# Kernel tuning notes

Measured on AMD Instinct MI355X. Metric: run time of the kernel, lower is better.

The kernel has to match this reference:

```python
import jax, jax.numpy as jnp
import numpy as np

B, C_IN, C_OUT, H, W, K, NK = 16, 256, 256, 64, 64, 3, 2
EPS = 1e-8


def setup_inputs() -> dict:
    key = jax.random.key(0)
    k1, k2, k3, k4 = jax.random.split(key, 4)
    x = jax.random.normal(k1, (B, C_IN, H, W), dtype=jnp.float32)
    mod = jax.random.normal(k2, (B, C_IN), dtype=jnp.float32)
    kernel_mod = jax.random.normal(k3, (B, NK), dtype=jnp.float32)
    # kernel bank: [num_conv_kernels, dim_out, dim_in, k, k] (kaiming-ish scale)
    weights = jax.random.normal(k4, (NK, C_OUT, C_IN, K, K), dtype=jnp.float32) / np.sqrt(C_IN * K * K)
    gamma = jnp.ones((C_OUT,), dtype=jnp.float32)
    return {"x": x, "mod": mod, "kernel_mod": kernel_mod, "weights": weights, "gamma": gamma}


def _block(x, mod, kernel_mod, weights, gamma):
    # adaptive kernel selection: softmax-mix the kernel bank per sample
    attn = jax.nn.softmax(kernel_mod, axis=-1)                       # [b, n]
    w = jnp.einsum('bn,noikl->boikl', attn, weights)                 # [b, o, i, k, k]
    # style modulation over input channels
    w = w * (mod[:, None, :, None, None] + 1.0)
    # demodulation
    denom = jnp.clip(jnp.sum(w * w, axis=(2, 3, 4), keepdims=True), EPS)
    w = w * jax.lax.rsqrt(denom)
    # per-sample conv (groups=b trick in torch) -> vmap over batch
    def conv_one(fmap, wb):
        return jax.lax.conv_general_dilated(
            fmap[None], wb, window_strides=(1, 1), padding='SAME',
            dimension_numbers=('NCHW', 'OIHW', 'NCHW'))[0]
    y = jax.vmap(conv_one)(x, w)                                     # [b, o, h, w]
    # RMSNorm over channel dim: F.normalize(x, dim=1) * gamma * sqrt(dim)
    norm = jnp.sqrt(jnp.sum(y * y, axis=1, keepdims=True))
    y = y / jnp.maximum(norm, 1e-12)
    y = y * gamma[None, :, None, None] * (gamma.shape[0] ** 0.5)
    # SiLU
    return y * jax.nn.sigmoid(y)


def reference(x, mod, kernel_mod, weights, gamma):
    return _block(x, mod, kernel_mod, weights, gamma)
```

## Files before the change

kernel.cpp:

```cpp
#include <hip/hip_runtime.h>
#include <math.h>


typedef __attribute__((ext_vector_type(8))) short short8;
typedef __attribute__((ext_vector_type(4))) float f32x4;

#define GLL16(src, dst)                                                       \
  __builtin_amdgcn_global_load_lds(                                           \
      (const __attribute__((address_space(1))) unsigned int*)(src),           \
      (__attribute__((address_space(3))) unsigned int*)(dst), 16, 0, 0)

static __device__ __forceinline__ unsigned short f2bf(float v) {
  union { float f; unsigned u; } u;
  u.f = v;
  unsigned r = u.u + 0x7FFF + ((u.u >> 16) & 1);
  return (unsigned short)(r >> 16);
}

__global__ __launch_bounds__(256) void scale_kernel(
    const float* __restrict__ mod, const float* __restrict__ kmod,
    const float* __restrict__ weights, float* __restrict__ scale) {
  int bo = blockIdx.x;
  int b = bo >> 8, o = bo & 255;

  float k0 = kmod[b * 2 + 0], k1 = kmod[b * 2 + 1];
  float mx = fmaxf(k0, k1);
  float e0 = expf(k0 - mx), e1 = expf(k1 - mx);
  float ai = 1.0f / (e0 + e1);
  float a0 = e0 * ai, a1 = e1 * ai;

  int t = threadIdx.x;
  const float* w0 = weights + (size_t)o * 2304;
  const float* w1 = w0 + 589824;

  float s = 0.0f;
#pragma unroll
  for (int r = 0; r < 9; r++) {
    int idx = t + r * 256;
    int i = idx / 9;
    float wv = a0 * w0[idx] + a1 * w1[idx];
    wv *= (mod[b * 256 + i] + 1.0f);
    s += wv * wv;
  }
#pragma unroll
  for (int off = 32; off > 0; off >>= 1) s += __shfl_down(s, off);

  __shared__ float red[4];
  if ((t & 63) == 0) red[t >> 6] = s;
  __syncthreads();
  if (t == 0) {
    float tot = red[0] + red[1] + red[2] + red[3];
    scale[bo] = rsqrtf(fmaxf(tot, 1e-8f));
  }
}

__global__ __launch_bounds__(256) void wprep(
    const float* __restrict__ mod, const float* __restrict__ kmod,
    const float* __restrict__ weights, const float* __restrict__ scale,
    unsigned short* __restrict__ wq) {
  __shared__ __align__(16) unsigned short buf[20480];
  int blk = blockIdx.x;
  int b = blk >> 5, ot = (blk >> 4) & 1, c = blk & 15;
  int t = threadIdx.x;

  float k0 = kmod[b * 2 + 0], k1 = kmod[b * 2 + 1];
  float mx = fmaxf(k0, k1);
  float e0 = expf(k0 - mx), e1 = expf(k1 - mx);
  float ai = 1.0f / (e0 + e1);
  float a0 = e0 * ai, a1 = e1 * ai;

#pragma unroll
  for (int k = 0; k < 8; ++k) {
    int e = t + k * 256;
    int half = e >> 10;
    buf[(half * 10 + 9) * 1024 + (e & 1023)] = 0;
  }

  int ol = t >> 1, eh = t & 1;
  int o = ot * 128 + ol;
  float sc = scale[b * 256 + o];
#pragma unroll
  for (int io = 0; io < 2; ++io) {
#pragma unroll
    for (int eo = 0; eo < 4; ++eo) {
      int e = eh * 4 + eo;
      int i = c * 16 + io * 8 + e;
      float f = (mod[b * 256 + i] + 1.0f) * sc;
      const float* w0 = &weights[((size_t)o * 256 + i) * 9];
      const float* w1 = w0 + 589824;
#pragma unroll
      for (int j = 0; j < 9; ++j) {
        float v = (a0 * w0[j] + a1 * w1[j]) * f;
        buf[(io * 10 + j) * 1024 + ol * 8 + e] = f2bf(v);
      }
    }
  }
  __syncthreads();
  size_t base = (size_t)blk * 20480;
#pragma unroll
  for (int k = 0; k < 10; ++k) {
    int idx = t + k * 256;
    *(short8*)(wq + base + (size_t)idx * 8) = *(const short8*)&buf[idx * 8];
  }
}

__global__ __launch_bounds__(256) void xprep(
    const float* __restrict__ x, unsigned short* __restrict__ xq) {
  int blk = blockIdx.x;
  int rowp = blk % 66;
  int bc = blk / 66;
  int b = bc >> 4, c = bc & 15;
  int t = threadIdx.x;
  size_t obase = (size_t)blk * 1056;

  if (rowp == 0 || rowp == 65) {
    for (int idx = t; idx < 1056; idx += 256) xq[obase + idx] = 0;
    return;
  }
  __shared__ __align__(16) unsigned short xs2[1056];
  int row = rowp - 1;
  for (int idx = t; idx < 1056; idx += 256) xs2[idx] = 0;
  __syncthreads();
#pragma unroll
  for (int k = 0; k < 4; ++k) {
    int idx = t + k * 256;
    int il = idx >> 6, col = idx & 63;
    float v = x[(((size_t)b * 256 + c * 16 + il) * 64 + row) * 64 + col];
    xs2[(col + 1) * 16 + il] = f2bf(v);
  }
  __syncthreads();
  if (t < 132) {
    int G = blk * 132 + t;
    int flip = ((G >> 3) & 1) ^ (bc & 1);
    *(short8*)(xq + obase + (size_t)(t ^ flip) * 8) = *(const short8*)&xs2[t * 8];
  }
}

__global__ __launch_bounds__(512, 2) void conv_mfma(
    const unsigned short* __restrict__ xq, const unsigned short* __restrict__ wq,
    float* __restrict__ out) {
  __shared__ __align__(16) unsigned short wsm[2][20480];
  __shared__ __align__(16) unsigned short xsm[2][10560];

  int bid = blockIdx.x;
  int xcd = bid & 7;
  int kk = bid >> 3;
  int b = xcd * 2 + (kk >> 4);
  int rem = kk & 15;
  int ot = rem >> 3;
  int rt = rem & 7;
  int r0 = rt * 8;

  int t = threadIdx.x;
  int w = t >> 6, lane = t & 63;
  int g = (t >> 4) & 3, lm = t & 15;

  int baddr_[5], aaddr_[5];
#pragma unroll
  for (int s = 0; s < 5; ++s) {
    int p = 4 * s + g;
    int io = (p >= 10) ? 1 : 0;
    int j = p - 10 * io;
    int jd3, jm3;
    if (j == 9) { jd3 = 0; jm3 = 0; }
    else { jd3 = (j >= 3) + (j >= 6); jm3 = j - 3 * jd3; }
    int ba = ((w + jd3) * 66 + lm + jm3) * 32 + io * 16;
    ba ^= ((ba >> 7) & 1) << 4;
    baddr_[s] = ba;
    aaddr_[s] = p * 2048 + lm * 16;
  }

  f32x4 acc[8][4];
#pragma unroll
  for (int mf = 0; mf < 8; ++mf)
#pragma unroll
    for (int nf = 0; nf < 4; ++nf) acc[mf][nf] = (f32x4){0.f, 0.f, 0.f, 0.f};

#define WGLL(cn, nb, r)                                                        \
  {                                                                            \
    const unsigned short* s_ = wq + ((size_t)(b * 32 + ot * 16 + (cn))) * 20480 \
                               + ((r) * 512 + w * 64 + lane) * 8;              \
    GLL16(s_, &wsm[nb][(r) * 4096 + w * 512]);                                 \
  }
#define XGLL(cn, nb, r)                                                        \
  {                                                                            \
    const unsigned short* s_ = xq + ((size_t)((b * 16 + (cn)) * 66 + r0)) * 1056 \
                               + ((r) * 512 + w * 64 + lane) * 8;              \
    GLL16(s_, &xsm[nb][(r) * 4096 + w * 512]);                                 \
  }

  WGLL(0, 0, 0); WGLL(0, 0, 1); WGLL(0, 0, 2); WGLL(0, 0, 3); WGLL(0, 0, 4);
  XGLL(0, 0, 0); XGLL(0, 0, 1);
  if (t < 296) XGLL(0, 0, 2);
  asm volatile("s_waitcnt vmcnt(0)" ::: "memory");
  __builtin_amdgcn_s_barrier();
  __builtin_amdgcn_sched_barrier(0);

  for (int c = 0; c < 16; ++c) {
    int cur = c & 1;
    const char* wsb = (const char*)wsm[cur];
    const char* xsb = (const char*)xsm[cur];
#pragma unroll
    for (int s = 0; s < 5; ++s) {
      if (c < 15) {
        int nb = cur ^ 1;
        if (s == 0) { WGLL(c + 1, nb, 0); WGLL(c + 1, nb, 1); XGLL(c + 1, nb, 0); }
        if (s == 1) { WGLL(c + 1, nb, 2); WGLL(c + 1, nb, 3); XGLL(c + 1, nb, 1); }
        if (s == 2) { WGLL(c + 1, nb, 4); if (t < 296) XGLL(c + 1, nb, 2); }
      }
      short8 A[8];
#pragma unroll
      for (int mf = 0; mf < 8; ++mf)
        A[mf] = *(const short8*)(wsb + aaddr_[s] + mf * 256);
      __builtin_amdgcn_s_setprio(1);
#pragma unroll
      for (int nf = 0; nf < 4; ++nf) {
        short8 Bf = *(const short8*)(xsb + baddr_[s] + nf * 512);
#pragma unroll
        for (int mf = 0; mf < 8; ++mf)
          acc[mf][nf] =
              __builtin_amdgcn_mfma_f32_16x16x32_bf16(A[mf], Bf, acc[mf][nf], 0, 0, 0);
      }
      __builtin_amdgcn_s_setprio(0);
    }
    asm volatile("s_waitcnt vmcnt(0)" ::: "memory");
    __builtin_amdgcn_s_barrier();
    __builtin_amdgcn_sched_barrier(0);
  }

  int row = r0 + w;
#pragma unroll
  for (int mf = 0; mf < 8; ++mf)
#pragma unroll
    for (int nf = 0; nf < 4; ++nf)
#pragma unroll
      for (int q = 0; q < 4; ++q) {
        int o = ot * 128 + mf * 16 + g * 4 + q;
        int col = nf * 16 + lm;
        out[(((size_t)b * 256 + o) * 64 + row) * 64 + col] = acc[mf][nf][q];
      }
#undef WGLL
#undef XGLL
}

__global__ __launch_bounds__(256) void norm_kernel(
    float* __restrict__ y, const float* __restrict__ gamma) {
  int blk = blockIdx.x;
  int b = blk >> 6, h = blk & 63;
  int t = threadIdx.x;
  int p = t & 63, og = t >> 6;

  size_t base = (((size_t)b * 256) * 64 + h) * 64 + p;
  float yv[64];
  float s = 0.0f;
#pragma unroll
  for (int k = 0; k < 64; k++) {
    yv[k] = y[base + (size_t)(og * 64 + k) * 4096];
    s = fmaf(yv[k], yv[k], s);
  }

  __shared__ float red[4][64];
  __shared__ float invs[64];
  red[og][p] = s;
  __syncthreads();
  if (og == 0) {
    float tot = red[0][p] + red[1][p] + red[2][p] + red[3][p];
    float nrm = sqrtf(tot);
    invs[p] = 16.0f / fmaxf(nrm, 1e-12f);
  }
  __syncthreads();
  float iv = invs[p];
#pragma unroll
  for (int k = 0; k < 64; k++) {
    int o = og * 64 + k;
    float v = yv[k] * iv * gamma[o];
    float sg = 1.0f / (1.0f + expf(-v));
    y[base + (size_t)o * 4096] = v * sg;
  }
}

extern "C" void kernel_launch(void* const* d_in, const int* in_sizes, int n_in,
                              void* d_out, int out_size, void* d_ws, size_t ws_size,
                              hipStream_t stream) {
  const float* x = (const float*)d_in[0];
  const float* mod = (const float*)d_in[1];
  const float* kmod = (const float*)d_in[2];
  const float* weights = (const float*)d_in[3];
  const float* gamma = (const float*)d_in[4];
  float* out = (float*)d_out;

  unsigned short* wq = (unsigned short*)d_ws;
  float* scale = (float*)((char*)d_ws + 20971520);
  unsigned short* xq = (unsigned short*)((char*)d_ws + 20987904);

  scale_kernel<<<16 * 256, 256, 0, stream>>>(mod, kmod, weights, scale);
  wprep<<<512, 256, 0, stream>>>(mod, kmod, weights, scale, wq);
  xprep<<<16 * 16 * 66, 256, 0, stream>>>(x, xq);
  conv_mfma<<<256, 512, 0, stream>>>(xq, wq, out);
  norm_kernel<<<16 * 64, 256, 0, stream>>>(out, gamma);
}
```

Baseline: 142.3 us.

## Fuse demod scale into weight prep and software-pipeline LDS reads in conv loop

```diff
diff --git a/kernel.cpp b/kernel.cpp
--- a/kernel.cpp
+++ b/kernel.cpp
@@ -17,11 +17,14 @@
   return (unsigned short)(r >> 16);
 }
 
-__global__ __launch_bounds__(256) void scale_kernel(
+__global__ __launch_bounds__(256) void wprep(
     const float* __restrict__ mod, const float* __restrict__ kmod,
-    const float* __restrict__ weights, float* __restrict__ scale) {
-  int bo = blockIdx.x;
-  int b = bo >> 8, o = bo & 255;
+    const float* __restrict__ weights, unsigned short* __restrict__ wq) {
+  int blk = blockIdx.x;
+  int b = blk >> 5, oq = blk & 31;
+  int t = threadIdx.x;
+  int o_l = t >> 5, its = t & 31;
+  int o = oq * 8 + o_l;
 
   float k0 = kmod[b * 2 + 0], k1 = kmod[b * 2 + 1];
   float mx = fmaxf(k0, k1);
@@ -29,78 +32,51 @@
   float ai = 1.0f / (e0 + e1);
   float a0 = e0 * ai, a1 = e1 * ai;
 
-  int t = threadIdx.x;
-  const float* w0 = weights + (size_t)o * 2304;
+  float wv[9][8];
+  float s = 0.0f;
+  const float* w0 = &weights[((size_t)o * 256 + its * 8) * 9];
   const float* w1 = w0 + 589824;
-
-  float s = 0.0f;
-#pragma unroll
-  for (int r = 0; r < 9; r++) {
-    int idx = t + r * 256;
-    int i = idx / 9;
-    float wv = a0 * w0[idx] + a1 * w1[idx];
-    wv *= (mod[b * 256 + i] + 1.0f);
-    s += wv * wv;
-  }
-#pragma unroll
-  for (int off = 32; off > 0; off >>= 1) s += __shfl_down(s, off);
-
-  __shared__ float red[4];
-  if ((t & 63) == 0) red[t >> 6] = s;
-  __syncthreads();
-  if (t == 0) {
-    float tot = red[0] + red[1] + red[2] + red[3];
-    scale[bo] = rsqrtf(fmaxf(tot, 1e-8f));
-  }
-}
-
-__global__ __launch_bounds__(256) void wprep(
-    const float* __restrict__ mod, const float* __restrict__ kmod,
-    const float* __restrict__ weights, const float* __restrict__ scale,
-    unsigned short* __restrict__ wq) {
-  __shared__ __align__(16) unsigned short buf[20480];
-  int blk = blockIdx.x;
-  int b = blk >> 5, ot = (blk >> 4) & 1, c = blk & 15;
-  int t = threadIdx.x;
-
-  float k0 = kmod[b * 2 + 0], k1 = kmod[b * 2 + 1];
-  float mx = fmaxf(k0, k1);
-  float e0 = expf(k0 - mx), e1 = expf(k1 - mx);
-  float ai = 1.0f / (e0 + e1);
-  float a0 = e0 * ai, a1 = e1 * ai;
-
-#pragma unroll
-  for (int k = 0; k < 8; ++k) {
-    int e = t + k * 256;
-    int half = e >> 10;
-    buf[(half * 10 + 9) * 1024 + (e & 1023)] = 0;
-  }
-
-  int ol = t >> 1, eh = t & 1;
-  int o = ot * 128 + ol;
-  float sc = scale[b * 256 + o];
-#pragma unroll
-  for (int io = 0; io < 2; ++io) {
-#pragma unroll
-    for (int eo = 0; eo < 4; ++eo) {
-      int e = eh * 4 + eo;
-      int i = c * 16 + io * 8 + e;
-      float f = (mod[b * 256 + i] + 1.0f) * sc;
-      const float* w0 = &weights[((size_t)o * 256 + i) * 9];
-      const float* w1 = w0 + 589824;
-#pragma unroll
-      for (int j = 0; j < 9; ++j) {
-        float v = (a0 * w0[j] + a1 * w1[j]) * f;
-        buf[(io * 10 + j) * 1024 + ol * 8 + e] = f2bf(v);
-      }
+#pragma unroll
+  for (int e = 0; e < 8; ++e) {
+    float f = mod[b * 256 + its * 8 + e] + 1.0f;
+#pragma unroll
+    for (int j = 0; j < 9; ++j) {
+      float v = (a0 * w0[e * 9 + j] + a1 * w1[e * 9 + j]) * f;
+      wv[j][e] = v;
+      s = fmaf(v, v, s);
     }
   }
-  __syncthreads();
-  size_t base = (size_t)blk * 20480;
-#pragma unroll
-  for (int k = 0; k < 10; ++k) {
-    int idx = t + k * 256;
-    *(short8*)(wq + base + (size_t)idx * 8) = *(const short8*)&buf[idx * 8];
+
+  __shared__ float red[8][32];
+  __shared__ float scl[8];
+  red[o_l][its] = s;
+  __syncthreads();
+  if (t < 8) {
+    float tot = 0.0f;
+#pragma unroll
+    for (int k = 0; k < 32; ++k) tot += red[t][k];
+    scl[t] = rsqrtf(fmaxf(tot, 1e-8f));
+  }
+  __syncthreads();
+  float sc = scl[o_l];
+
+  int c = its >> 1, io = its & 1;
+  int ot = o >> 7, ol = o & 127;
+  size_t base = ((size_t)(b * 32 + ot * 16 + c)) * 20480 + ol * 8;
+#pragma unroll
+  for (int j = 0; j < 9; ++j) {
+    short8 pk;
+#pragma unroll
+    for (int e = 0; e < 8; ++e) pk[e] = (short)f2bf(wv[j][e] * sc);
+    *(short8*)(wq + base + (io * 10 + j) * 1024) = pk;
+  }
+  {
+    int c2 = t >> 4, io2 = (t >> 3) & 1, olq = t & 7;
+    int o2 = oq * 8 + olq;
+    int ot2 = o2 >> 7, olz = o2 & 127;
+    short8 z = {0, 0, 0, 0, 0, 0, 0, 0};
+    *(short8*)(wq + ((size_t)(b * 32 + ot2 * 16 + c2)) * 20480 +
+               (io2 * 10 + 9) * 1024 + olz * 8) = z;
   }
 }
 
@@ -176,56 +152,102 @@
 #pragma unroll
     for (int nf = 0; nf < 4; ++nf) acc[mf][nf] = (f32x4){0.f, 0.f, 0.f, 0.f};
 
-#define WGLL(cn, nb, r)                                                        \
-  {                                                                            \
-    const unsigned short* s_ = wq + ((size_t)(b * 32 + ot * 16 + (cn))) * 20480 \
-                               + ((r) * 512 + w * 64 + lane) * 8;              \
-    GLL16(s_, &wsm[nb][(r) * 4096 + w * 512]);                                 \
-  }
-#define XGLL(cn, nb, r)                                                        \
-  {                                                                            \
+#define WGLL(cn, nb, r)                                                          \
+  {                                                                              \
+    const unsigned short* s_ = wq + ((size_t)(b * 32 + ot * 16 + (cn))) * 20480  \
+                               + ((r) * 512 + w * 64 + lane) * 8;                \
+    GLL16(s_, &wsm[nb][(r) * 4096 + w * 512]);                                   \
+  }
+#define XGLL(cn, nb, r)                                                          \
+  {                                                                              \
     const unsigned short* s_ = xq + ((size_t)((b * 16 + (cn)) * 66 + r0)) * 1056 \
-                               + ((r) * 512 + w * 64 + lane) * 8;              \
-    GLL16(s_, &xsm[nb][(r) * 4096 + w * 512]);                                 \
-  }
+                               + ((r) * 512 + w * 64 + lane) * 8;                \
+    GLL16(s_, &xsm[nb][(r) * 4096 + w * 512]);                                   \
+  }
+
+  short8 PA[8], PB[4], QA[8], QB[4];
+
+#define DSRD(SA, SB_, cbuf, s)                                                  \
+  {                                                                             \
+    const char* wsb_ = (const char*)wsm[cbuf];                                  \
+    const char* xsb_ = (const char*)xsm[cbuf];                                  \
+    _Pragma("unroll")                                                           \
+    for (int mf = 0; mf < 8; ++mf)                                              \
+      SA[mf] = *(const short8*)(wsb_ + aaddr_[s] + mf * 256);                   \
+    _Pragma("unroll")                                                           \
+    for (int nf = 0; nf < 4; ++nf)                                              \
+      SB_[nf] = *(const short8*)(xsb_ + baddr_[s] + nf * 512);                  \
+  }
+
+#define MFMA32(SA, SB_)                                                         \
+  {                                                                             \
+    __builtin_amdgcn_s_setprio(1);                                              \
+    _Pragma("unroll")                                                           \
+    for (int nf = 0; nf < 4; ++nf)                                              \
+      _Pragma("unroll")                                                         \
+      for (int mf = 0; mf < 8; ++mf)                                            \
+        acc[mf][nf] = __builtin_amdgcn_mfma_f32_16x16x32_bf16(                  \
+            SA[mf], SB_[nf], acc[mf][nf], 0, 0, 0);                             \
+    __builtin_amdgcn_s_setprio(0);                                              \
+  }
+
+#define SBAR __builtin_amdgcn_sched_barrier(0)
+#define LGKM0 asm volatile("s_waitcnt lgkmcnt(0)" ::: "memory")
+#define VM0 asm volatile("s_waitcnt vmcnt(0)" ::: "memory")
 
   WGLL(0, 0, 0); WGLL(0, 0, 1); WGLL(0, 0, 2); WGLL(0, 0, 3); WGLL(0, 0, 4);
   XGLL(0, 0, 0); XGLL(0, 0, 1);
   if (t < 296) XGLL(0, 0, 2);
-  asm volatile("s_waitcnt vmcnt(0)" ::: "memory");
+  VM0;
   __builtin_amdgcn_s_barrier();
-  __builtin_amdgcn_sched_barrier(0);
-
-  for (int c = 0; c < 16; ++c) {
-    int cur = c & 1;
-    const char* wsb = (const char*)wsm[cur];
-    const char* xsb = (const char*)xsm[cur];
-#pragma unroll
-    for (int s = 0; s < 5; ++s) {
-      if (c < 15) {
-        int nb = cur ^ 1;
-        if (s == 0) { WGLL(c + 1, nb, 0); WGLL(c + 1, nb, 1); XGLL(c + 1, nb, 0); }
-        if (s == 1) { WGLL(c + 1, nb, 2); WGLL(c + 1, nb, 3); XGLL(c + 1, nb, 1); }
-        if (s == 2) { WGLL(c + 1, nb, 4); if (t < 296) XGLL(c + 1, nb, 2); }
-      }
-      short8 A[8];
-#pragma unroll
-      for (int mf = 0; mf < 8; ++mf)
-        A[mf] = *(const short8*)(wsb + aaddr_[s] + mf * 256);
-      __builtin_amdgcn_s_setprio(1);
-#pragma unroll
-      for (int nf = 0; nf < 4; ++nf) {
-        short8 Bf = *(const short8*)(xsb + baddr_[s] + nf * 512);
-#pragma unroll
-        for (int mf = 0; mf < 8; ++mf)
-          acc[mf][nf] =
-              __builtin_amdgcn_mfma_f32_16x16x32_bf16(A[mf], Bf, acc[mf][nf], 0, 0, 0);
-      }
-      __builtin_amdgcn_s_setprio(0);
+  SBAR;
+  DSRD(PA, PB, 0, 0);
+
+  for (int cc = 0; cc < 16; cc += 2) {
+    DSRD(QA, QB, 0, 1); WGLL(cc + 1, 1, 0); WGLL(cc + 1, 1, 1); SBAR;
+    MFMA32(PA, PB);
+    DSRD(PA, PB, 0, 2); WGLL(cc + 1, 1, 2); WGLL(cc + 1, 1, 3); SBAR;
+    MFMA32(QA, QB);
+    DSRD(QA, QB, 0, 3); WGLL(cc + 1, 1, 4); XGLL(cc + 1, 1, 0); SBAR;
+    MFMA32(PA, PB);
+    DSRD(PA, PB, 0, 4); XGLL(cc + 1, 1, 1);
+    if (t < 296) XGLL(cc + 1, 1, 2);
+    SBAR;
+    MFMA32(QA, QB);
+    LGKM0; SBAR;
+    VM0;
+    __builtin_amdgcn_s_barrier();
+    SBAR;
+    DSRD(QA, QB, 1, 0); SBAR;
+    MFMA32(PA, PB);
+    if (cc < 14) {
+      DSRD(PA, PB, 1, 1); WGLL(cc + 2, 0, 0); WGLL(cc + 2, 0, 1); SBAR;
+      MFMA32(QA, QB);
+      DSRD(QA, QB, 1, 2); WGLL(cc + 2, 0, 2); WGLL(cc + 2, 0, 3); SBAR;
+      MFMA32(PA, PB);
+      DSRD(PA, PB, 1, 3); WGLL(cc + 2, 0, 4); XGLL(cc + 2, 0, 0); SBAR;
+      MFMA32(QA, QB);
+      DSRD(QA, QB, 1, 4); XGLL(cc + 2, 0, 1);
+      if (t < 296) XGLL(cc + 2, 0, 2);
+      SBAR;
+      MFMA32(PA, PB);
+      LGKM0; SBAR;
+      VM0;
+      __builtin_amdgcn_s_barrier();
+      SBAR;
+      DSRD(PA, PB, 0, 0); SBAR;
+      MFMA32(QA, QB);
+    } else {
+      DSRD(PA, PB, 1, 1); SBAR;
+      MFMA32(QA, QB);
+      DSRD(QA, QB, 1, 2); SBAR;
+      MFMA32(PA, PB);
+      DSRD(PA, PB, 1, 3); SBAR;
+      MFMA32(QA, QB);
+      DSRD(QA, QB, 1, 4); SBAR;
+      MFMA32(PA, PB);
+      MFMA32(QA, QB);
     }
-    asm volatile("s_waitcnt vmcnt(0)" ::: "memory");
-    __builtin_amdgcn_s_barrier();
-    __builtin_amdgcn_sched_barrier(0);
   }
 
   int row = r0 + w;
@@ -241,6 +263,11 @@
       }
 #undef WGLL
 #undef XGLL
+#undef DSRD
+#undef MFMA32
+#undef SBAR
+#undef LGKM0
+#undef VM0
 }
 
 __global__ __launch_bounds__(256) void norm_kernel(
@@ -290,11 +317,9 @@
   float* out = (float*)d_out;
 
   unsigned short* wq = (unsigned short*)d_ws;
-  float* scale = (float*)((char*)d_ws + 20971520);
   unsigned short* xq = (unsigned short*)((char*)d_ws + 20987904);
 
-  scale_kernel<<<16 * 256, 256, 0, stream>>>(mod, kmod, weights, scale);
-  wprep<<<512, 256, 0, stream>>>(mod, kmod, weights, scale, wq);
+  wprep<<<512, 256, 0, stream>>>(mod, kmod, weights, wq);
   xprep<<<16 * 16 * 66, 256, 0, stream>>>(x, xq);
   conv_mfma<<<256, 512, 0, stream>>>(xq, wq, out);
   norm_kernel<<<16 * 64, 256, 0, stream>>>(out, gamma);
```

After: 453.4 us. 3.19x slower.
